# Kernel tuning notes

Hardware: AMD Instinct MI355X
Metric: run time of the kernel (lower is better)

Reference implementation:

```python
import jax, jax.numpy as jnp
import numpy as np

D_MODEL = 1024
N_HEADS = 16
HEAD_DIM = D_MODEL // N_HEADS  # 64
WINDOW = 64
HALF = WINDOW // 2  # query i attends keys in [i-HALF, i+HALF]
CHUNK = WINDOW      # chunk size for banded attention; must be >= HALF and divide S
B, S = 4, 4096


def setup_inputs() -> dict:
    key = jax.random.key(0)
    ks = jax.random.split(key, 6)
    s = 0.02
    D = D_MODEL
    return {
        "x":  jax.random.normal(ks[0], (B, S, D), jnp.float32),
        "Wq": jax.random.normal(ks[1], (D, D), jnp.float32) * s,
        "bq": jnp.zeros((D,), jnp.float32),
        "Wk": jax.random.normal(ks[2], (D, D), jnp.float32) * s,
        "bk": jnp.zeros((D,), jnp.float32),
        "Wv": jax.random.normal(ks[3], (D, D), jnp.float32) * s,
        "bv": jnp.zeros((D,), jnp.float32),
        "Wo": jax.random.normal(ks[4], (D, D), jnp.float32) * s,
        "bo": jnp.zeros((D,), jnp.float32),
    }


def reference(x, Wq, bq, Wk, bk, Wv, bv, Wo, bo):
    # Sliding-window attention (seq_len > 128 path of SparseAttention).
    b, s, d = x.shape
    h, hd = N_HEADS, HEAD_DIM
    scale = 1.0 / np.sqrt(hd).astype(np.float32)

    q = (x @ Wq.T + bq).reshape(b, s, h, hd)
    k = (x @ Wk.T + bk).reshape(b, s, h, hd)
    v = (x @ Wv.T + bv).reshape(b, s, h, hd)

    c = CHUNK
    nb = s // c
    qc = q.reshape(b, nb, c, h, hd)

    # Pad one chunk of zeros on each side; each query chunk attends keys in
    # chunks [n-1, n, n+1] (covers the +/-HALF band since HALF <= c).
    pad = jnp.zeros((b, c, h, hd), q.dtype)
    kp = jnp.concatenate([pad, k, pad], axis=1).reshape(b, nb + 2, c, h, hd)
    vp = jnp.concatenate([pad, v, pad], axis=1).reshape(b, nb + 2, c, h, hd)
    k3 = jnp.concatenate([kp[:, :-2], kp[:, 1:-1], kp[:, 2:]], axis=2)  # [b,nb,3c,h,hd]
    v3 = jnp.concatenate([vp[:, :-2], vp[:, 1:-1], vp[:, 2:]], axis=2)

    # scores: [b,h,nb,c,3c]
    scores = jnp.einsum('bnqhd,bnkhd->bhnqk', qc, k3) * scale

    # Banded validity mask. Global query pos = n*c + i ; global key pos = n*c + j - c.
    i = jnp.arange(c)[:, None]          # [c,1]
    j = jnp.arange(3 * c)[None, :]      # [1,3c]
    rel = j - c - i                     # key_pos - query_pos, [c,3c]
    band = (rel >= -HALF) & (rel <= HALF)
    n = jnp.arange(nb)[:, None, None]   # [nb,1,1]
    keypos = n * c + (j - c)[None, :, :]  # [nb,1,3c]
    valid = band[None, :, :] & (keypos >= 0) & (keypos < s)  # [nb,c,3c]

    attn = jax.nn.softmax(jnp.where(valid[None, None], scores, -jnp.inf), axis=-1)
    ctx = jnp.einsum('bhnqk,bnkhd->bnqhd', attn, v3).reshape(b, s, d)
    return ctx @ Wo.T + bo
```

## Files before the change

kernel.cpp:

```cpp
#include <hip/hip_runtime.h>
#include <hip/hip_bf16.h>
#include <cstdint>
#include <cstddef>

#define D_MODEL 1024
#define NHEADS  16
#define HDIM    64
#define HALFW   32
#define BATCH   4
#define SEQ     4096
#define MROWS   (BATCH*SEQ)

typedef __attribute__((ext_vector_type(8))) short        bf16x8;
typedef __attribute__((ext_vector_type(4))) float        f32x4;
typedef __attribute__((ext_vector_type(4))) unsigned int u32x4;

typedef const __attribute__((address_space(1))) void gvoid_t;
typedef __attribute__((address_space(3))) void       lvoid_t;

__device__ __forceinline__ unsigned short f2bf(float f) {
    unsigned int u = __float_as_uint(f);
    u += 0x7fffu + ((u >> 16) & 1u);
    return (unsigned short)(u >> 16);
}

__device__ __forceinline__ int vswz(int row, int bytecol) {
    return (row * 256 + bytecol) ^ (((row ^ (row >> 3)) & 7) << 4);
}

__global__ __launch_bounds__(256)
void cvt_f32_bf16(const float* __restrict__ src, unsigned short* __restrict__ dst, int n8) {
    int i = blockIdx.x * 256 + threadIdx.x;
    if (i >= n8) return;
    float4 a = *(const float4*)(src + (size_t)i * 8);
    float4 b = *(const float4*)(src + (size_t)i * 8 + 4);
    u32x4 o;
    o[0] = (unsigned)f2bf(a.x) | ((unsigned)f2bf(a.y) << 16);
    o[1] = (unsigned)f2bf(a.z) | ((unsigned)f2bf(a.w) << 16);
    o[2] = (unsigned)f2bf(b.x) | ((unsigned)f2bf(b.y) << 16);
    o[3] = (unsigned)f2bf(b.z) | ((unsigned)f2bf(b.w) << 16);
    *(u32x4*)(dst + (size_t)i * 8) = o;
}

__global__ __launch_bounds__(256)
void cvt4_f32_bf16(const float* __restrict__ s0, const float* __restrict__ s1,
                   const float* __restrict__ s2, const float* __restrict__ s3,
                   unsigned short* __restrict__ d0, unsigned short* __restrict__ d1,
                   unsigned short* __restrict__ d2, unsigned short* __restrict__ d3, int n8) {
    int i = blockIdx.x * 256 + threadIdx.x;
    if (i >= n8) return;
    const float* src = blockIdx.y == 0 ? s0 : blockIdx.y == 1 ? s1 : blockIdx.y == 2 ? s2 : s3;
    unsigned short* dst = blockIdx.y == 0 ? d0 : blockIdx.y == 1 ? d1 : blockIdx.y == 2 ? d2 : d3;
    float4 a = *(const float4*)(src + (size_t)i * 8);
    float4 b = *(const float4*)(src + (size_t)i * 8 + 4);
    u32x4 o;
    o[0] = (unsigned)f2bf(a.x) | ((unsigned)f2bf(a.y) << 16);
    o[1] = (unsigned)f2bf(a.z) | ((unsigned)f2bf(a.w) << 16);
    o[2] = (unsigned)f2bf(b.x) | ((unsigned)f2bf(b.y) << 16);
    o[3] = (unsigned)f2bf(b.z) | ((unsigned)f2bf(b.w) << 16);
    *(u32x4*)(dst + (size_t)i * 8) = o;
}

template <int NOUT, int F32OUT>
__global__ __launch_bounds__(512)
void gemm256(const unsigned short* __restrict__ A,
             const unsigned short* __restrict__ W0,
             const unsigned short* __restrict__ W1,
             const unsigned short* __restrict__ W2,
             const float* __restrict__ b0, const float* __restrict__ b1,
             const float* __restrict__ b2,
             unsigned short* __restrict__ o0, unsigned short* __restrict__ o1,
             unsigned short* __restrict__ o2, float* __restrict__ of32)
{
    constexpr int K  = 1024;
    constexpr int NT = K / 32;
    constexpr int NWG = 64 * 4 * NOUT;
    __shared__ unsigned short lds[65536];

    const int tid  = threadIdx.x;
    const int wave = tid >> 6, lane = tid & 63;
    const int wr = wave >> 2, wc = wave & 3;

    const int bid = blockIdx.x;
    const int g   = (bid & 7) * (NWG / 8) + (bid >> 3);
    const int rb  = g / (4 * NOUT);
    const int cb  = g % (4 * NOUT);
    const int which = cb >> 2;
    const int bm = rb * 256, bn = (cb & 3) * 256;

    const unsigned short* W = (NOUT == 1 || which == 0) ? W0 : (which == 1 ? W1 : W2);
    const float* bias       = (NOUT == 1 || which == 0) ? b0 : (which == 1 ? b1 : b2);
    unsigned short* obf     = (NOUT == 1 || which == 0) ? o0 : (which == 1 ? o1 : o2);

    f32x4 acc[8][4];
    #pragma unroll
    for (int m = 0; m < 8; ++m)
        #pragma unroll
        for (int n = 0; n < 4; ++n)
            #pragma unroll
            for (int j = 0; j < 4; ++j) acc[m][n][j] = 0.0f;

    const int r0  = tid >> 2;
    const int ks0 = ((tid & 3) - (r0 >> 1)) & 3;
    const size_t aoff0 = (size_t)(bm + r0)       * K + ks0 * 8;
    const size_t aoff1 = (size_t)(bm + r0 + 128) * K + ks0 * 8;
    const size_t boff0 = (size_t)(bn + r0)       * K + ks0 * 8;
    const size_t boff1 = (size_t)(bn + r0 + 128) * K + ks0 * 8;
    const int stW = wave * 1024;

    char* ldsb = (char*)lds;

    auto STAGE_A = [&](int t) {
        const int slot = (t & 3) * 32768;
        const int kt = t * 32;
        __builtin_amdgcn_global_load_lds((gvoid_t*)(A + aoff0 + kt),
            (lvoid_t*)(ldsb + slot + stW), 16, 0, 0);
        __builtin_amdgcn_global_load_lds((gvoid_t*)(A + aoff1 + kt),
            (lvoid_t*)(ldsb + slot + 8192 + stW), 16, 0, 0);
    };
    auto STAGE_B = [&](int t) {
        const int slot = (t & 3) * 32768 + 16384;
        const int kt = t * 32;
        __builtin_amdgcn_global_load_lds((gvoid_t*)(W + boff0 + kt),
            (lvoid_t*)(ldsb + slot + stW), 16, 0, 0);
        __builtin_amdgcn_global_load_lds((gvoid_t*)(W + boff1 + kt),
            (lvoid_t*)(ldsb + slot + 8192 + stW), 16, 0, 0);
    };

    const int lr  = lane & 15;
    const int xb_ = (((lane >> 4) + (lr >> 1)) & 3) << 4;
    const int aread = (wr * 128 + lr) * 64 + xb_;
    const int bread = 16384 + (wc * 64 + lr) * 64 + xb_;

    STAGE_A(0); STAGE_B(0); STAGE_A(1); STAGE_B(1); STAGE_A(2); STAGE_B(2);
    asm volatile("s_waitcnt vmcnt(8)" ::: "memory");
    __builtin_amdgcn_s_barrier();

    for (int t = 0; t < NT; ++t) {
        const char* sl = ldsb + (t & 3) * 32768;
        bf16x8 a_lo[4], bfr[4];
        #pragma unroll
        for (int m = 0; m < 4; ++m)
            a_lo[m] = *(const bf16x8*)(sl + aread + m * 1024);
        #pragma unroll
        for (int n = 0; n < 4; ++n)
            bfr[n] = *(const bf16x8*)(sl + bread + n * 1024);
        if (t + 3 < NT) STAGE_A(t + 3);
        __builtin_amdgcn_s_barrier();
        __builtin_amdgcn_s_setprio(1);
        #pragma unroll
        for (int m = 0; m < 4; ++m)
            #pragma unroll
            for (int n = 0; n < 4; ++n)
                acc[m][n] = __builtin_amdgcn_mfma_f32_16x16x32_bf16(a_lo[m], bfr[n], acc[m][n], 0, 0, 0);
        __builtin_amdgcn_s_setprio(0);
        __builtin_amdgcn_s_barrier();
        bf16x8 a_hi[4];
        #pragma unroll
        for (int m = 0; m < 4; ++m)
            a_hi[m] = *(const bf16x8*)(sl + aread + 4096 + m * 1024);
        if (t + 3 < NT) {
            STAGE_B(t + 3);
            asm volatile("s_waitcnt vmcnt(8)" ::: "memory");
        } else if (t == NT - 3) {
            asm volatile("s_waitcnt vmcnt(4)" ::: "memory");
        } else if (t == NT - 2) {
            asm volatile("s_waitcnt vmcnt(0)" ::: "memory");
        }
        __builtin_amdgcn_s_barrier();
        __builtin_amdgcn_s_setprio(1);
        #pragma unroll
        for (int m = 0; m < 4; ++m)
            #pragma unroll
            for (int n = 0; n < 4; ++n)
                acc[m + 4][n] = __builtin_amdgcn_mfma_f32_16x16x32_bf16(a_hi[m], bfr[n], acc[m + 4][n], 0, 0, 0);
        __builtin_amdgcn_s_setprio(0);
        __builtin_amdgcn_s_barrier();
    }

    float bvv[4];
    #pragma unroll
    for (int n = 0; n < 4; ++n) bvv[n] = bias[bn + wc * 64 + n * 16 + lr];
    #pragma unroll
    for (int m = 0; m < 8; ++m) {
        #pragma unroll
        for (int j = 0; j < 4; ++j) {
            const int row = bm + wr * 128 + m * 16 + (lane >> 4) * 4 + j;
            #pragma unroll
            for (int n = 0; n < 4; ++n) {
                const int col = bn + wc * 64 + n * 16 + lr;
                const float v = acc[m][n][j] + bvv[n];
                if (F32OUT) of32[(size_t)row * 1024 + col] = v;
                else        obf[(size_t)row * 1024 + col]  = f2bf(v);
            }
        }
    }
}

__global__ __launch_bounds__(256)
void attn_band(const unsigned short* __restrict__ Q,
               const unsigned short* __restrict__ Kk,
               const unsigned short* __restrict__ V,
               unsigned short* __restrict__ Ctx)
{
    __shared__ unsigned short Qs[64 * 72];
    __shared__ unsigned short Ks[128 * 72];
    __shared__ unsigned short Vt[64 * 128];
    __shared__ unsigned short Ps[64 * 128];

    const int qt = blockIdx.x, h = blockIdx.y, b = blockIdx.z;
    const int qbase  = qt * 64;
    const int kstart = qbase - HALFW;
    const int tid = threadIdx.x, wave = tid >> 6, lane = tid & 63;

    const size_t base = (size_t)b * SEQ * D_MODEL + (size_t)h * HDIM;
    const unsigned short* Qb = Q  + base;
    const unsigned short* Kb = Kk + base;
    const unsigned short* Vb = V  + base;
    unsigned short*       Cb = Ctx + base;

    for (int c = tid; c < 512; c += 256) {
        const int row = c >> 3, col = (c & 7) * 8;
        *(u32x4*)(Qs + row * 72 + col) =
            *(const u32x4*)(Qb + (size_t)(qbase + row) * D_MODEL + col);
    }
    for (int c = tid; c < 1024; c += 256) {
        const int krow = c >> 3, col = (c & 7) * 8;
        const int kpos = kstart + krow;
        u32x4 kv;
        if (kpos >= 0 && kpos < SEQ) {
            kv = *(const u32x4*)(Kb + (size_t)kpos * D_MODEL + col);
        } else {
            for (int j = 0; j < 4; ++j) kv[j] = 0u;
        }
        *(u32x4*)(Ks + krow * 72 + col) = kv;
    }
    for (int c = tid; c < 512; c += 256) {
        const int p = c >> 3, dch = c & 7;
        const int k0 = kstart + 2 * p, k1 = k0 + 1;
        u32x4 v0, v1;
        if (k0 >= 0 && k0 < SEQ) {
            v0 = *(const u32x4*)(Vb + (size_t)k0 * D_MODEL + dch * 8);
        } else {
            for (int j = 0; j < 4; ++j) v0[j] = 0u;
        }
        if (k1 >= 0 && k1 < SEQ) {
            v1 = *(const u32x4*)(Vb + (size_t)k1 * D_MODEL + dch * 8);
        } else {
            for (int j = 0; j < 4; ++j) v1[j] = 0u;
        }
        #pragma unroll
        for (int j = 0; j < 8; ++j) {
            const int d = dch * 8 + j;
            const unsigned lo = (v0[j >> 1] >> ((j & 1) * 16)) & 0xffffu;
            const unsigned hi = (v1[j >> 1] >> ((j & 1) * 16)) & 0xffffu;
            *(unsigned*)((char*)Vt + vswz(d, 4 * p)) = lo | (hi << 16);
        }
    }
    __syncthreads();

    f32x4 sc[8];
    #pragma unroll
    for (int c = 0; c < 8; ++c)
        #pragma unroll
        for (int j = 0; j < 4; ++j) sc[c][j] = 0.0f;

    bf16x8 aq[2];
    #pragma unroll
    for (int kc = 0; kc < 2; ++kc)
        aq[kc] = *(const bf16x8*)(Qs + (wave * 16 + (lane & 15)) * 72 + kc * 32 + (lane >> 4) * 8);
    #pragma unroll
    for (int c = 0; c < 8; ++c) {
        #pragma unroll
        for (int kc = 0; kc < 2; ++kc) {
            bf16x8 bk_ = *(const bf16x8*)(Ks + (c * 16 + (lane & 15)) * 72 + kc * 32 + (lane >> 4) * 8);
            sc[c] = __builtin_amdgcn_mfma_f32_16x16x32_bf16(aq[kc], bk_, sc[c], 0, 0, 0);
        }
    }

    const int grp = lane >> 4, colk = lane & 15;
    float rowmax[4] = {-1e30f, -1e30f, -1e30f, -1e30f};
    #pragma unroll
    for (int c = 0; c < 8; ++c) {
        const int kpos = kstart + c * 16 + colk;
        #pragma unroll
        for (int j = 0; j < 4; ++j) {
            const int qpos = qbase + wave * 16 + grp * 4 + j;
            const int rel = kpos - qpos;
            const bool valid = (kpos >= 0) && (kpos < SEQ) && (rel >= -HALFW) && (rel <= HALFW);
            const float v = valid ? sc[c][j] * 0.125f : -1e30f;
            sc[c][j] = v;
            rowmax[j] = fmaxf(rowmax[j], v);
        }
    }
    #pragma unroll
    for (int j = 0; j < 4; ++j)
        #pragma unroll
        for (int m = 1; m < 16; m <<= 1)
            rowmax[j] = fmaxf(rowmax[j], __shfl_xor(rowmax[j], m, 64));

    float rowsum[4] = {0.f, 0.f, 0.f, 0.f};
    #pragma unroll
    for (int c = 0; c < 8; ++c)
        #pragma unroll
        for (int j = 0; j < 4; ++j) {
            const float p = __expf(sc[c][j] - rowmax[j]);
            sc[c][j] = p;
            rowsum[j] += p;
        }
    #pragma unroll
    for (int j = 0; j < 4; ++j)
        #pragma unroll
        for (int m = 1; m < 16; m <<= 1)
            rowsum[j] += __shfl_xor(rowsum[j], m, 64);

    #pragma unroll
    for (int c = 0; c < 8; ++c)
        #pragma unroll
        for (int j = 0; j < 4; ++j)
            *(unsigned short*)((char*)Ps + vswz(wave * 16 + grp * 4 + j, (c * 16 + colk) * 2))
                = f2bf(sc[c][j]);
    __syncthreads();

    f32x4 o[4];
    #pragma unroll
    for (int n = 0; n < 4; ++n)
        #pragma unroll
        for (int j = 0; j < 4; ++j) o[n][j] = 0.0f;
    #pragma unroll
    for (int kc = 0; kc < 4; ++kc) {
        bf16x8 pa = *(const bf16x8*)((const char*)Ps +
                        vswz(wave * 16 + (lane & 15), kc * 64 + (lane >> 4) * 16));
        #pragma unroll
        for (int n = 0; n < 4; ++n) {
            bf16x8 bv_ = *(const bf16x8*)((const char*)Vt +
                            vswz(n * 16 + (lane & 15), kc * 64 + (lane >> 4) * 16));
            o[n] = __builtin_amdgcn_mfma_f32_16x16x32_bf16(pa, bv_, o[n], 0, 0, 0);
        }
    }

    float rinv[4];
    #pragma unroll
    for (int j = 0; j < 4; ++j) rinv[j] = 1.0f / rowsum[j];
    #pragma unroll
    for (int n = 0; n < 4; ++n)
        #pragma unroll
        for (int j = 0; j < 4; ++j) {
            const int q = qbase + wave * 16 + grp * 4 + j;
            Cb[(size_t)q * D_MODEL + n * 16 + colk] = f2bf(o[n][j] * rinv[j]);
        }
}

extern "C" void kernel_launch(void* const* d_in, const int* in_sizes, int n_in,
                              void* d_out, int out_size, void* d_ws, size_t ws_size,
                              hipStream_t stream)
{
    (void)in_sizes; (void)n_in; (void)out_size; (void)ws_size;
    const float* x  = (const float*)d_in[0];
    const float* Wq = (const float*)d_in[1];
    const float* bq = (const float*)d_in[2];
    const float* Wk = (const float*)d_in[3];
    const float* bk = (const float*)d_in[4];
    const float* Wv = (const float*)d_in[5];
    const float* bv = (const float*)d_in[6];
    const float* Wo = (const float*)d_in[7];
    const float* bo = (const float*)d_in[8];
    float* out = (float*)d_out;

    char* ws = (char*)d_ws;
    unsigned short* xb  = (unsigned short*)ws;
    unsigned short* wqb = (unsigned short*)(ws + 33554432);
    unsigned short* wkb = wqb + 1048576;
    unsigned short* wvb = wkb + 1048576;
    unsigned short* wob = wvb + 1048576;
    unsigned short* qb  = wob + 1048576;
    unsigned short* kb  = qb + (size_t)MROWS * D_MODEL;
    unsigned short* vb  = kb + (size_t)MROWS * D_MODEL;
    unsigned short* ctxb = xb;

    cvt_f32_bf16<<<dim3(MROWS * D_MODEL / 8 / 256), 256, 0, stream>>>(x, xb, MROWS * D_MODEL / 8);
    cvt4_f32_bf16<<<dim3(D_MODEL * D_MODEL / 8 / 256, 4), 256, 0, stream>>>(
        Wq, Wk, Wv, Wo, wqb, wkb, wvb, wob, D_MODEL * D_MODEL / 8);

    gemm256<3, 0><<<dim3(768), 512, 0, stream>>>(
        xb, wqb, wkb, wvb, bq, bk, bv, qb, kb, vb, nullptr);

    attn_band<<<dim3(SEQ / 64, NHEADS, BATCH), 256, 0, stream>>>(qb, kb, vb, ctxb);

    gemm256<1, 1><<<dim3(256), 512, 0, stream>>>(
        ctxb, wob, wob, wob, bo, bo, bo, nullptr, nullptr, nullptr, out);
}
```

Before: 232.7 us.

## Restructure GEMM mainloop to K=64 steps with A/B split LDS ring

Rewrites the bf16 GEMM main loop to step K by 64, split into two 32-wide halves. A and B now sit in separate 4-slot LDS rings (A at offset 0, B at 64KB), and prefetch runs one stage ahead instead of three. Each half loads all 8 A fragments once and streams B in two pairs, with global-to-LDS staging interleaved between MFMA phases. The aim is fewer barriers and waitcnts per unit of work and better reuse of A fragments from registers. The cost is a shallower prefetch distance and a higher register count for the A fragments.

```diff
diff --git a/kernel.cpp b/kernel.cpp
--- a/kernel.cpp
+++ b/kernel.cpp
@@ -73,7 +73,7 @@
              unsigned short* __restrict__ o2, float* __restrict__ of32)
 {
     constexpr int K  = 1024;
-    constexpr int NT = K / 32;
+    constexpr int NT = K / 64;
     constexpr int NWG = 64 * 4 * NOUT;
     __shared__ unsigned short lds[65536];
 
@@ -100,82 +100,107 @@
             #pragma unroll
             for (int j = 0; j < 4; ++j) acc[m][n][j] = 0.0f;
 
-    const int r0  = tid >> 2;
-    const int ks0 = ((tid & 3) - (r0 >> 1)) & 3;
-    const size_t aoff0 = (size_t)(bm + r0)       * K + ks0 * 8;
-    const size_t aoff1 = (size_t)(bm + r0 + 128) * K + ks0 * 8;
-    const size_t boff0 = (size_t)(bn + r0)       * K + ks0 * 8;
-    const size_t boff1 = (size_t)(bn + r0 + 128) * K + ks0 * 8;
-    const int stW = wave * 1024;
-
     char* ldsb = (char*)lds;
 
-    auto STAGE_A = [&](int t) {
-        const int slot = (t & 3) * 32768;
-        const int kt = t * 32;
-        __builtin_amdgcn_global_load_lds((gvoid_t*)(A + aoff0 + kt),
-            (lvoid_t*)(ldsb + slot + stW), 16, 0, 0);
-        __builtin_amdgcn_global_load_lds((gvoid_t*)(A + aoff1 + kt),
-            (lvoid_t*)(ldsb + slot + 8192 + stW), 16, 0, 0);
+    const int idx0 = tid, idx1 = tid + 512;
+    const int r0 = idx0 >> 2, r1 = idx1 >> 2;
+    const int c0 = ((idx0 & 3) - (r0 >> 1)) & 3;
+    const int c1 = ((idx1 & 3) - (r1 >> 1)) & 3;
+    const size_t sA0 = (size_t)(bm + r0) * K + c0 * 8;
+    const size_t sA1 = (size_t)(bm + r1) * K + c1 * 8;
+    const size_t sB0 = (size_t)(bn + r0) * K + c0 * 8;
+    const size_t sB1 = (size_t)(bn + r1) * K + c1 * 8;
+    const int ldsW = wave * 1024;
+
+    auto STAGE = [&](int t, int kh, int isA) {
+        const int slot = ((t << 1) + kh) & 3;
+        const int base = (isA ? 0 : 65536) + slot * 16384 + ldsW;
+        const int ke = t * 64 + kh * 32;
+        const unsigned short* M = isA ? A : W;
+        const size_t s0 = isA ? sA0 : sB0;
+        const size_t s1 = isA ? sA1 : sB1;
+        __builtin_amdgcn_global_load_lds((gvoid_t*)(M + s0 + ke),
+            (lvoid_t*)(ldsb + base), 16, 0, 0);
+        __builtin_amdgcn_global_load_lds((gvoid_t*)(M + s1 + ke),
+            (lvoid_t*)(ldsb + base + 8192), 16, 0, 0);
     };
-    auto STAGE_B = [&](int t) {
-        const int slot = (t & 3) * 32768 + 16384;
-        const int kt = t * 32;
-        __builtin_amdgcn_global_load_lds((gvoid_t*)(W + boff0 + kt),
-            (lvoid_t*)(ldsb + slot + stW), 16, 0, 0);
-        __builtin_amdgcn_global_load_lds((gvoid_t*)(W + boff1 + kt),
-            (lvoid_t*)(ldsb + slot + 8192 + stW), 16, 0, 0);
-    };
-
-    const int lr  = lane & 15;
-    const int xb_ = (((lane >> 4) + (lr >> 1)) & 3) << 4;
-    const int aread = (wr * 128 + lr) * 64 + xb_;
-    const int bread = 16384 + (wc * 64 + lr) * 64 + xb_;
-
-    STAGE_A(0); STAGE_B(0); STAGE_A(1); STAGE_B(1); STAGE_A(2); STAGE_B(2);
-    asm volatile("s_waitcnt vmcnt(8)" ::: "memory");
+
+    const int lr = lane & 15;
+    const int pp = (((lane >> 4) + (lr >> 1)) & 3) << 4;
+    const int abase = (wr * 128 + lr) * 64 + pp;
+    const int bbase = 65536 + (wc * 64 + lr) * 64 + pp;
+
+    STAGE(0, 0, 1); STAGE(0, 0, 0); STAGE(0, 1, 1); STAGE(0, 1, 0);
+    asm volatile("s_waitcnt vmcnt(4)" ::: "memory");
     __builtin_amdgcn_s_barrier();
 
+    #pragma unroll 1
     for (int t = 0; t < NT; ++t) {
-        const char* sl = ldsb + (t & 3) * 32768;
-        bf16x8 a_lo[4], bfr[4];
-        #pragma unroll
-        for (int m = 0; m < 4; ++m)
-            a_lo[m] = *(const bf16x8*)(sl + aread + m * 1024);
-        #pragma unroll
-        for (int n = 0; n < 4; ++n)
-            bfr[n] = *(const bf16x8*)(sl + bread + n * 1024);
-        if (t + 3 < NT) STAGE_A(t + 3);
-        __builtin_amdgcn_s_barrier();
-        __builtin_amdgcn_s_setprio(1);
-        #pragma unroll
-        for (int m = 0; m < 4; ++m)
-            #pragma unroll
-            for (int n = 0; n < 4; ++n)
-                acc[m][n] = __builtin_amdgcn_mfma_f32_16x16x32_bf16(a_lo[m], bfr[n], acc[m][n], 0, 0, 0);
-        __builtin_amdgcn_s_setprio(0);
-        __builtin_amdgcn_s_barrier();
-        bf16x8 a_hi[4];
-        #pragma unroll
-        for (int m = 0; m < 4; ++m)
-            a_hi[m] = *(const bf16x8*)(sl + aread + 4096 + m * 1024);
-        if (t + 3 < NT) {
-            STAGE_B(t + 3);
-            asm volatile("s_waitcnt vmcnt(8)" ::: "memory");
-        } else if (t == NT - 3) {
-            asm volatile("s_waitcnt vmcnt(4)" ::: "memory");
-        } else if (t == NT - 2) {
-            asm volatile("s_waitcnt vmcnt(0)" ::: "memory");
-        }
-        __builtin_amdgcn_s_barrier();
-        __builtin_amdgcn_s_setprio(1);
-        #pragma unroll
-        for (int m = 0; m < 4; ++m)
-            #pragma unroll
-            for (int n = 0; n < 4; ++n)
-                acc[m + 4][n] = __builtin_amdgcn_mfma_f32_16x16x32_bf16(a_hi[m], bfr[n], acc[m + 4][n], 0, 0, 0);
-        __builtin_amdgcn_s_setprio(0);
-        __builtin_amdgcn_s_barrier();
+        const int more = (t + 1 < NT);
+        {
+            const int so = (((t << 1) + 0) & 3) * 16384;
+            if (more) STAGE(t + 1, 0, 1);
+            bf16x8 a[8], b2_[2];
+            #pragma unroll
+            for (int m = 0; m < 8; ++m) a[m] = *(const bf16x8*)(ldsb + so + abase + m * 1024);
+            #pragma unroll
+            for (int n = 0; n < 2; ++n) b2_[n] = *(const bf16x8*)(ldsb + so + bbase + n * 1024);
+            __builtin_amdgcn_s_barrier();
+            __builtin_amdgcn_s_setprio(1);
+            #pragma unroll
+            for (int m = 0; m < 8; ++m)
+                #pragma unroll
+                for (int n = 0; n < 2; ++n)
+                    acc[m][n] = __builtin_amdgcn_mfma_f32_16x16x32_bf16(a[m], b2_[n], acc[m][n], 0, 0, 0);
+            __builtin_amdgcn_s_setprio(0);
+            __builtin_amdgcn_s_barrier();
+            if (more) STAGE(t + 1, 0, 0);
+            #pragma unroll
+            for (int n = 0; n < 2; ++n) b2_[n] = *(const bf16x8*)(ldsb + so + bbase + (n + 2) * 1024);
+            __builtin_amdgcn_s_barrier();
+            __builtin_amdgcn_s_setprio(1);
+            #pragma unroll
+            for (int m = 0; m < 8; ++m)
+                #pragma unroll
+                for (int n = 0; n < 2; ++n)
+                    acc[m][n + 2] = __builtin_amdgcn_mfma_f32_16x16x32_bf16(a[m], b2_[n], acc[m][n + 2], 0, 0, 0);
+            __builtin_amdgcn_s_setprio(0);
+            if (more) { asm volatile("s_waitcnt vmcnt(4)" ::: "memory"); }
+            else      { asm volatile("s_waitcnt vmcnt(0)" ::: "memory"); }
+            __builtin_amdgcn_s_barrier();
+        }
+        {
+            const int so = (((t << 1) + 1) & 3) * 16384;
+            if (more) STAGE(t + 1, 1, 1);
+            bf16x8 a[8], b2_[2];
+            #pragma unroll
+            for (int m = 0; m < 8; ++m) a[m] = *(const bf16x8*)(ldsb + so + abase + m * 1024);
+            #pragma unroll
+            for (int n = 0; n < 2; ++n) b2_[n] = *(const bf16x8*)(ldsb + so + bbase + n * 1024);
+            __builtin_amdgcn_s_barrier();
+            __builtin_amdgcn_s_setprio(1);
+            #pragma unroll
+            for (int m = 0; m < 8; ++m)
+                #pragma unroll
+                for (int n = 0; n < 2; ++n)
+                    acc[m][n] = __builtin_amdgcn_mfma_f32_16x16x32_bf16(a[m], b2_[n], acc[m][n], 0, 0, 0);
+            __builtin_amdgcn_s_setprio(0);
+            __builtin_amdgcn_s_barrier();
+            if (more) STAGE(t + 1, 1, 0);
+            #pragma unroll
+            for (int n = 0; n < 2; ++n) b2_[n] = *(const bf16x8*)(ldsb + so + bbase + (n + 2) * 1024);
+            __builtin_amdgcn_s_barrier();
+            __builtin_amdgcn_s_setprio(1);
+            #pragma unroll
+            for (int m = 0; m < 8; ++m)
+                #pragma unroll
+                for (int n = 0; n < 2; ++n)
+                    acc[m][n + 2] = __builtin_amdgcn_mfma_f32_16x16x32_bf16(a[m], b2_[n], acc[m][n + 2], 0, 0, 0);
+            __builtin_amdgcn_s_setprio(0);
+            if (t + 2 < NT) { asm volatile("s_waitcnt vmcnt(4)" ::: "memory"); }
+            else            { asm volatile("s_waitcnt vmcnt(0)" ::: "memory"); }
+            __builtin_amdgcn_s_barrier();
+        }
     }
 
     float bvv[4];
```

Result: no change. 232.2 us (-0.2%).
